# Kernel optimization log

Measured on AMD Instinct MI355X. Metric: run time of the kernel, lower is better.

The kernel has to match this reference:

```python
import jax, jax.numpy as jnp
import numpy as np

NUM_HEADS_LIST = [8, 16]
HIDDEN_SIZE_LIST = [1024, 2048]
NUM_HEADS_KV = 8
MAX_HIDDEN = max(HIDDEN_SIZE_LIST)
B, T = 4, 1024
NEG = -1e9


def _rope_cos_sin(position_ids, head_dim, dtype):
    # HF-style RoPE: inv_freq over even dims, emb = cat(freqs, freqs)
    inv_freq = 1.0 / (10000.0 ** (jnp.arange(0, head_dim, 2, dtype=jnp.float32) / head_dim))
    freqs = position_ids.astype(jnp.float32)[..., None] * inv_freq  # (B,T,d/2)
    emb = jnp.concatenate([freqs, freqs], axis=-1)                  # (B,T,d)
    # unsqueeze head dim -> (B,1,T,d)
    return jnp.cos(emb).astype(dtype)[:, None], jnp.sin(emb).astype(dtype)[:, None]


def _rotate_half(x):
    d = x.shape[-1] // 2
    return jnp.concatenate([-x[..., d:], x[..., :d]], axis=-1)


def setup_inputs() -> dict:
    key = jax.random.key(0)
    k1, k2, k3, k4 = jax.random.split(key, 4)
    q_m = jax.random.normal(k1, (B, T, MAX_HIDDEN), dtype=jnp.float32)
    k_m = jax.random.normal(k2, (B, T, MAX_HIDDEN), dtype=jnp.float32)
    v_m = jax.random.normal(k3, (B, T, MAX_HIDDEN), dtype=jnp.float32)
    weights = jax.random.uniform(k4, (len(NUM_HEADS_LIST) * len(HIDDEN_SIZE_LIST),), dtype=jnp.float32)
    weights = weights / jnp.sum(weights)
    causal = jnp.tril(jnp.ones((T, T), dtype=bool))
    attention_mask = jnp.broadcast_to(
        jnp.where(causal, 0.0, NEG).astype(jnp.float32)[None, None], (B, 1, T, T)
    )
    position_ids = jnp.broadcast_to(jnp.arange(T, dtype=jnp.int64)[None], (B, T))
    return {"q_m": q_m, "k_m": k_m, "v_m": v_m, "weights": weights,
            "attention_mask": attention_mask, "position_ids": position_ids}


def reference(q_m, k_m, v_m, weights, attention_mask, position_ids):
    b, t, _ = q_m.shape
    dtype = q_m.dtype
    out = jnp.zeros((b, t, MAX_HIDDEN), dtype)
    l = 0
    for h in NUM_HEADS_LIST:
        d_max = MAX_HIDDEN // h  # padded head dim for this head-count config
        q_mix = jnp.zeros((b, h, t, d_max), dtype)
        k_mix = jnp.zeros((b, NUM_HEADS_KV, t, d_max), dtype)
        v_mix = jnp.zeros((b, NUM_HEADS_KV, t, d_max), dtype)
        for e in HIDDEN_SIZE_LIST:
            d = e // h
            q = q_m[:, :, :e].reshape(b, t, h, d).transpose(0, 2, 1, 3)                  # (b,h,t,d)
            k = k_m[:, :, :d * NUM_HEADS_KV].reshape(b, t, NUM_HEADS_KV, d).transpose(0, 2, 1, 3)
            v = v_m[:, :, :d * NUM_HEADS_KV].reshape(b, t, NUM_HEADS_KV, d).transpose(0, 2, 1, 3)
            cos, sin = _rope_cos_sin(position_ids, d, dtype)
            q = q * cos + _rotate_half(q) * sin
            k = k * cos + _rotate_half(k) * sin
            pad = ((0, 0), (0, 0), (0, 0), (0, d_max - d))
            w = weights[l]
            q_mix = q_mix + w * jnp.pad(q, pad)
            k_mix = k_mix + w * jnp.pad(k, pad)
            v_mix = v_mix + w * jnp.pad(v, pad)
            l += 1
        # GQA: repeat kv heads to match h
        n_rep = h // NUM_HEADS_KV
        kr = jnp.repeat(k_mix, n_rep, axis=1)
        vr = jnp.repeat(v_mix, n_rep, axis=1)
        scale = 1.0 / np.sqrt(d_max).astype(np.float32)
        scores = jnp.einsum('bhqd,bhkd->bhqk', q_mix, kr) * scale
        scores = scores + attention_mask[:, :, :, :t]
        att = jax.nn.softmax(scores, axis=-1)
        y = jnp.einsum('bhqk,bhkd->bhqd', att, vr)
        y = y.transpose(0, 2, 1, 3).reshape(b, t, h * d_max)  # h*d_max == MAX_HIDDEN
        out = out + y
    return out
```

## Files before the change

### kernel.cpp

```cpp
#include <hip/hip_runtime.h>
#include <math.h>

#define B_   4
#define T_   1024
#define MAXH 2048
#define NKV  8

typedef unsigned int uint;
typedef unsigned short ushort;
typedef __attribute__((ext_vector_type(8))) short bf16x8;
typedef __attribute__((ext_vector_type(4))) float f32x4;

__device__ __forceinline__ ushort f2bf(float f) {
    uint u = __float_as_uint(f);
    u += 0x7fffu + ((u >> 16) & 1u);
    return (ushort)(u >> 16);
}

template<int H1>
__global__ __launch_bounds__(256) void mixqk_fused(
    const float* __restrict__ src, ushort* __restrict__ dst0,
    ushort* __restrict__ dst1, const float* __restrict__ wts)
{
    __shared__ float L[2048];
    const int bt = blockIdx.x;
    const int t = bt & (T_ - 1), b = bt >> 10;
    const float* row = src + (size_t)bt * MAXH;
    const int tid = threadIdx.x;
#pragma unroll
    for (int i = 0; i < 2; i++) {
        int idx = tid + i * 256;
        *(float4*)&L[idx * 4] = *(const float4*)&row[idx * 4];
    }
    __syncthreads();
    const float w0s = wts[0], w0b = wts[1], w1s = wts[2], w1b = wts[3];
    const float tf = (float)t;
    constexpr float LG = 13.287712379549449f;

#pragma unroll
    for (int i = 0; i < 4; i++) {
        int p = tid + i * 256;
        int hh = p >> 7, jh = p & 127;
        float ab = tf * exp2f((float)jh * (-2.f * LG / 256.f));
        float sb = __sinf(ab), cb = __cosf(ab);
        float x0 = L[hh * 256 + jh], x1 = L[hh * 256 + jh + 128];
        float v0 = w0b * (x0 * cb - x1 * sb);
        float v1 = w0b * (x1 * cb + x0 * sb);
        float as = tf * exp2f((float)(jh & 63) * (-2.f * LG / 128.f));
        float ss = __sinf(as), cs = __cosf(as);
        float y  = L[hh * 128 + jh];
        float yr = (jh < 64) ? -L[hh * 128 + jh + 64] : L[hh * 128 + jh - 64];
        v0 += w0s * (y * cs + yr * ss);
        ushort* d0 = dst0 + (((size_t)b * 8 + hh) * T_ + t) * 256;
        d0[jh] = f2bf(v0); d0[jh + 128] = f2bf(v1);
    }
#pragma unroll
    for (int i = 0; i < H1 / 4; i++) {
        int p = tid + i * 256;
        int h = p >> 6, jh = p & 63;
        float ab = tf * exp2f((float)jh * (-2.f * LG / 128.f));
        float sb = __sinf(ab), cb = __cosf(ab);
        float x0 = L[h * 128 + jh], x1 = L[h * 128 + jh + 64];
        float v0 = w1b * (x0 * cb - x1 * sb);
        float v1 = w1b * (x1 * cb + x0 * sb);
        float as = tf * exp2f((float)(jh & 31) * (-2.f * LG / 64.f));
        float ss = __sinf(as), cs = __cosf(as);
        float y  = L[h * 64 + jh];
        float yr = (jh < 32) ? -L[h * 64 + jh + 32] : L[h * 64 + jh - 32];
        v0 += w1s * (y * cs + yr * ss);
        ushort* d1 = dst1 + (((size_t)b * H1 + h) * T_ + t) * 128;
        d1[jh] = f2bf(v0); d1[jh + 64] = f2bf(v1);
    }
}

template<int DMAX>
__global__ __launch_bounds__(256) void mixv_t(
    const float* __restrict__ src, ushort* __restrict__ dst,
    const float* __restrict__ wts, int wsi, int wbi)
{
    constexpr int DS = DMAX / 2;
    constexpr int DDN = DMAX / 32;
    __shared__ ushort tile[32][33];
    int bid = blockIdx.x;
    int dd = bid % DDN;  bid /= DDN;
    int tt = bid & 31;   int bk = bid >> 5;
    int b = bk >> 3, kh = bk & 7;
    int tid = threadIdx.x;
    float wb = wts[wbi], wsm = wts[wsi];

    int jloc = tid & 31;
    int j = dd * 32 + jloc;
#pragma unroll
    for (int p = 0; p < 4; p++) {
        int tl = (tid >> 5) + p * 8;
        const float* row = src + ((size_t)b * T_ + tt * 32 + tl) * MAXH;
        float v = wb * row[kh * DMAX + j];
        if (j < DS) v += wsm * row[kh * DS + j];
        tile[tl][jloc] = f2bf(v);
    }
    __syncthreads();
    int tl = tid & 31;
#pragma unroll
    for (int p = 0; p < 4; p++) {
        int jl = (tid >> 5) + p * 8;
        dst[((size_t)bk * DMAX + dd * 32 + jl) * T_ + tt * 32 + tl] = tile[tl][jl];
    }
}

template<int NC, int NSUB, int RS, int NQ>
__device__ __forceinline__ void attn_inst(
    const bf16x8* qf, f32x4* acc, f32x4* accl, ushort* ps,
    const ushort* lds, int ksbase, int vtbase,
    float scale2, int qw, int kt32, int qtr, int l16)
{
    const bool full = (kt32 + 31) <= qw;
    f32x4 s0[NQ], s1[NQ];
#pragma unroll
    for (int qi = 0; qi < NQ; qi++) { s0[qi] = (f32x4){0.f,0.f,0.f,0.f}; s1[qi] = (f32x4){0.f,0.f,0.f,0.f}; }

    __builtin_amdgcn_s_setprio(1);
#pragma unroll
    for (int c = 0; c < NC; c++) {
        int ch = ((c * 4 + qtr) ^ (l16 & 7)) * 8;
        bf16x8 k0 = *(const bf16x8*)&lds[ksbase + l16 * RS + ch];
        bf16x8 k1 = *(const bf16x8*)&lds[ksbase + (16 + l16) * RS + ch];
#pragma unroll
        for (int qi = 0; qi < NQ; qi++) {
            s0[qi] = __builtin_amdgcn_mfma_f32_16x16x32_bf16(qf[qi * NC + c], k0, s0[qi], 0, 0, 0);
            s1[qi] = __builtin_amdgcn_mfma_f32_16x16x32_bf16(qf[qi * NC + c], k1, s1[qi], 0, 0, 0);
        }
    }
    __builtin_amdgcn_s_setprio(0);

    bf16x8 pa[NQ];
#pragma unroll
    for (int qi = 0; qi < NQ; qi++) {
        float p0[4], p1[4];
#pragma unroll
        for (int rr = 0; rr < 4; rr++) {
            p0[rr] = exp2f(s0[qi][rr] * scale2);
            p1[rr] = exp2f(s1[qi][rr] * scale2);
            if (!full) {
                int qq = qw + qtr * 4 + rr;
                if (kt32 + l16 > qq)      p0[rr] = 0.f;
                if (kt32 + 16 + l16 > qq) p1[rr] = 0.f;
            }
        }
#pragma unroll
        for (int rr = 0; rr < 4; rr++) {
            int row = qtr * 4 + rr;
            ps[row * 32 + (((l16 >> 3) ^ (row & 3)) * 8) + (l16 & 7)]       = f2bf(p0[rr]);
            ps[row * 32 + (((2 + (l16 >> 3)) ^ (row & 3)) * 8) + (l16 & 7)] = f2bf(p1[rr]);
        }
        pa[qi] = *(const bf16x8*)&ps[l16 * 32 + ((qtr ^ (l16 & 3)) * 8)];
    }

    bf16x8 ones;
#pragma unroll
    for (int j = 0; j < 8; j++) ones[j] = (short)0x3f80;
    __builtin_amdgcn_s_setprio(1);
#pragma unroll
    for (int s = 0; s < NSUB; s++) {
        bf16x8 vb = *(const bf16x8*)&lds[vtbase + (s * 16 + l16) * 40 + qtr * 8];
#pragma unroll
        for (int qi = 0; qi < NQ; qi++)
            acc[qi * NSUB + s] = __builtin_amdgcn_mfma_f32_16x16x32_bf16(pa[qi], vb, acc[qi * NSUB + s], 0, 0, 0);
    }
#pragma unroll
    for (int qi = 0; qi < NQ; qi++)
        accl[qi] = __builtin_amdgcn_mfma_f32_16x16x32_bf16(pa[qi], ones, accl[qi], 0, 0, 0);
    __builtin_amdgcn_s_setprio(0);
}

__global__ __launch_bounds__(512, 2) void attn_fused(
    const ushort* __restrict__ qmix0, const ushort* __restrict__ kmix0, const ushort* __restrict__ vt0,
    const ushort* __restrict__ qmix1, const ushort* __restrict__ kmix1, const ushort* __restrict__ vt1,
    float* __restrict__ out)
{
    __shared__ alignas(16) ushort lds[31744];
    constexpr int KS0 = 0, KS1 = 8192, VT0 = 12288, VT1 = 22528, PS = 27648;

    const int bid = blockIdx.x;
    const int half = bid >> 8;
    const int ipair = (bid >> 5) & 7;
    const int idx = bid & 31;
    const int b = idx >> 3, kh = idx & 7;
    const int qt = half ? ipair : 15 - ipair;

    const int tid = threadIdx.x;
    const int wid = tid >> 6, lane = tid & 63;
    const int qtr = lane >> 4, l16 = lane & 15;
    const int cfg = wid >> 2;
    const int w4 = wid & 3;

    const ushort* kg0 = kmix0 + ((size_t)b * NKV + kh) * T_ * 256;
    const ushort* vg0 = vt0   + ((size_t)b * NKV + kh) * 256 * T_;
    const ushort* kg1 = kmix1 + ((size_t)b * NKV + kh) * T_ * 128;
    const ushort* vg1 = vt1   + ((size_t)b * NKV + kh) * 128 * T_;

    const int k0r0 = tid >> 5,         k0c0 = tid & 31;
    const int k0r1 = (tid + 512) >> 5, k0c1 = (tid + 512) & 31;
    const int v0d0 = tid >> 2,         v0c0 = tid & 3;
    const int v0d1 = (tid + 512) >> 2, v0c1 = (tid + 512) & 3;
    const int k1r = tid >> 4, k1c = tid & 15;
    const int v1d = tid >> 2, v1c = tid & 3;

    ushort* ps = &lds[PS + wid * 512];

    const int nkt = 2 * qt + 2;
    const int qw = qt * 64 + w4 * 16;

    bf16x8 qf[8];
    if (cfg == 0) {
        const ushort* qb = qmix0 + (((size_t)b * 8 + kh) * T_ + qw + l16) * 256 + qtr * 8;
#pragma unroll
        for (int c = 0; c < 8; c++) qf[c] = *(const bf16x8*)(qb + c * 32);
    } else {
#pragma unroll
        for (int hI = 0; hI < 2; hI++) {
            const ushort* qb = qmix1 + (((size_t)b * 16 + 2 * kh + hI) * T_ + qw + l16) * 128 + qtr * 8;
#pragma unroll
            for (int c = 0; c < 4; c++) qf[hI * 4 + c] = *(const bf16x8*)(qb + c * 32);
        }
    }

    f32x4 acc[16];
    f32x4 accl[2] = {{0.f,0.f,0.f,0.f},{0.f,0.f,0.f,0.f}};
#pragma unroll
    for (int s = 0; s < 16; s++) acc[s] = (f32x4){0.f,0.f,0.f,0.f};

    const float scale2_0 = 0.0625f * 1.4426950408889634f;
    const float scale2_1 = 0.08838834764831845f * 1.4426950408889634f;

    uint4 k0a, k0b, v0a, v0b, k1a, v1a;
#define ISSUE(kt_) do {                                                              \
        k0a = *(const uint4*)(kg0 + (size_t)((kt_) * 32 + k0r0) * 256 + k0c0 * 8);   \
        k0b = *(const uint4*)(kg0 + (size_t)((kt_) * 32 + k0r1) * 256 + k0c1 * 8);   \
        v0a = *(const uint4*)(vg0 + (size_t)v0d0 * T_ + (kt_) * 32 + v0c0 * 8);      \
        v0b = *(const uint4*)(vg0 + (size_t)v0d1 * T_ + (kt_) * 32 + v0c1 * 8);      \
        k1a = *(const uint4*)(kg1 + (size_t)((kt_) * 32 + k1r) * 128 + k1c * 8);     \
        v1a = *(const uint4*)(vg1 + (size_t)v1d * T_ + (kt_) * 32 + v1c * 8);        \
    } while (0)

    ISSUE(0);
    for (int kt = 0; kt < nkt; kt++) {
        asm volatile("s_barrier" ::: "memory");
        *(uint4*)&lds[KS0 + k0r0 * 256 + ((k0c0 ^ (k0r0 & 7)) * 8)] = k0a;
        *(uint4*)&lds[KS0 + k0r1 * 256 + ((k0c1 ^ (k0r1 & 7)) * 8)] = k0b;
        *(uint4*)&lds[VT0 + v0d0 * 40 + v0c0 * 8] = v0a;
        *(uint4*)&lds[VT0 + v0d1 * 40 + v0c1 * 8] = v0b;
        *(uint4*)&lds[KS1 + k1r * 128 + ((k1c ^ (k1r & 7)) * 8)] = k1a;
        *(uint4*)&lds[VT1 + v1d * 40 + v1c * 8] = v1a;
        if (kt + 1 < nkt) ISSUE(kt + 1);
        asm volatile("s_waitcnt lgkmcnt(0)" ::: "memory");
        asm volatile("s_barrier" ::: "memory");

        const int kt32 = kt * 32;
        if (kt32 > qw + 15) continue;

        if (cfg == 0) {
            attn_inst<8, 16, 256, 1>(qf, acc, accl, ps, lds, KS0, VT0,
                                     scale2_0, qw, kt32, qtr, l16);
        } else {
            attn_inst<4, 8, 128, 2>(qf, acc, accl, ps, lds, KS1, VT1,
                                    scale2_1, qw, kt32, qtr, l16);
        }
    }
#undef ISSUE

    if (cfg == 0) {
        float linv[4];
#pragma unroll
        for (int rr = 0; rr < 4; rr++) linv[rr] = 1.f / accl[0][rr];
        float* ob = out + ((size_t)b * T_ + qw) * MAXH + kh * 256;
#pragma unroll
        for (int s = 0; s < 16; s++)
#pragma unroll
            for (int rr = 0; rr < 4; rr++)
                ob[(size_t)(qtr * 4 + rr) * MAXH + s * 16 + l16] = acc[s][rr] * linv[rr];
    }
    __syncthreads();
    if (cfg == 1) {
        float linva[4], linvb[4];
#pragma unroll
        for (int rr = 0; rr < 4; rr++) { linva[rr] = 1.f / accl[0][rr]; linvb[rr] = 1.f / accl[1][rr]; }
        float* ob = out + ((size_t)b * T_ + qw) * MAXH + kh * 256;
#pragma unroll
        for (int s = 0; s < 8; s++)
#pragma unroll
            for (int rr = 0; rr < 4; rr++)
                ob[(size_t)(qtr * 4 + rr) * MAXH + s * 16 + l16] += acc[s][rr] * linva[rr];
#pragma unroll
        for (int s = 0; s < 8; s++)
#pragma unroll
            for (int rr = 0; rr < 4; rr++)
                ob[(size_t)(qtr * 4 + rr) * MAXH + 128 + s * 16 + l16] += acc[8 + s][rr] * linvb[rr];
    }
}

extern "C" void kernel_launch(void* const* d_in, const int* in_sizes, int n_in,
                              void* d_out, int out_size, void* d_ws, size_t ws_size,
                              hipStream_t stream) {
    const float* q_m = (const float*)d_in[0];
    const float* k_m = (const float*)d_in[1];
    const float* v_m = (const float*)d_in[2];
    const float* wts = (const float*)d_in[3];
    float* out = (float*)d_out;
    ushort* ws = (ushort*)d_ws;

    ushort* qmix0 = ws;
    ushort* kmix0 = ws + 8388608u;
    ushort* vt0   = ws + 16777216u;
    ushort* qmix1 = ws + 25165824u;
    ushort* kmix1 = ws + 33554432u;
    ushort* vt1   = ws + 37748736u;

    dim3 blk(256);
    mixqk_fused<16><<<4096, blk, 0, stream>>>(q_m, qmix0, qmix1, wts);
    mixqk_fused<8><<<4096, blk, 0, stream>>>(k_m, kmix0, kmix1, wts);
    mixv_t<256><<<8192, blk, 0, stream>>>(v_m, vt0, wts, 0, 1);
    mixv_t<128><<<4096, blk, 0, stream>>>(v_m, vt1, wts, 2, 3);

    attn_fused<<<dim3(512), dim3(512), 0, stream>>>(qmix0, kmix0, vt0, qmix1, kmix1, vt1, out);
}
```

Baseline: 142.2 us.

## Split attention per config into separate blocks with atomic output accumulation, fuse prep kernels

Merges the four mixing/transposing kernels into one launch that also zeroes the output buffer. The attention kernel is split so each 256-thread block handles only one head-count config rather than both, doubling the grid to 1024 blocks and cutting LDS use to allow three blocks per CU. The two configs' contributions are combined with float atomic adds into the zeroed output instead of ordered writes. The V LDS pitch also shrinks from 40 to 36. This trades fewer launches and better occupancy against extra atomic traffic, an output zeroing pass, and nondeterministic summation order.

```diff
diff --git a/kernel.cpp b/kernel.cpp
--- a/kernel.cpp
+++ b/kernel.cpp
@@ -18,12 +18,10 @@
 }
 
 template<int H1>
-__global__ __launch_bounds__(256) void mixqk_fused(
-    const float* __restrict__ src, ushort* __restrict__ dst0,
-    ushort* __restrict__ dst1, const float* __restrict__ wts)
-{
-    __shared__ float L[2048];
-    const int bt = blockIdx.x;
+__device__ __forceinline__ void mixqk_body(
+    int bt, const float* __restrict__ src, ushort* __restrict__ dst0,
+    ushort* __restrict__ dst1, const float* __restrict__ wts, float* L)
+{
     const int t = bt & (T_ - 1), b = bt >> 10;
     const float* row = src + (size_t)bt * MAXH;
     const int tid = threadIdx.x;
@@ -74,14 +72,12 @@
 }
 
 template<int DMAX>
-__global__ __launch_bounds__(256) void mixv_t(
-    const float* __restrict__ src, ushort* __restrict__ dst,
-    const float* __restrict__ wts, int wsi, int wbi)
+__device__ __forceinline__ void mixv_body(
+    int bid, const float* __restrict__ src, ushort* __restrict__ dst,
+    const float* __restrict__ wts, int wsi, int wbi, ushort* tile )
 {
     constexpr int DS = DMAX / 2;
     constexpr int DDN = DMAX / 32;
-    __shared__ ushort tile[32][33];
-    int bid = blockIdx.x;
     int dd = bid % DDN;  bid /= DDN;
     int tt = bid & 31;   int bk = bid >> 5;
     int b = bk >> 3, kh = bk & 7;
@@ -96,18 +92,43 @@
         const float* row = src + ((size_t)b * T_ + tt * 32 + tl) * MAXH;
         float v = wb * row[kh * DMAX + j];
         if (j < DS) v += wsm * row[kh * DS + j];
-        tile[tl][jloc] = f2bf(v);
+        tile[tl * 33 + jloc] = f2bf(v);
     }
     __syncthreads();
     int tl = tid & 31;
 #pragma unroll
     for (int p = 0; p < 4; p++) {
         int jl = (tid >> 5) + p * 8;
-        dst[((size_t)bk * DMAX + dd * 32 + jl) * T_ + tt * 32 + tl] = tile[tl][jl];
-    }
-}
-
-template<int NC, int NSUB, int RS, int NQ>
+        dst[((size_t)bk * DMAX + dd * 32 + jl) * T_ + tt * 32 + tl] = tile[tl * 33 + jl];
+    }
+}
+
+__global__ __launch_bounds__(256) void mix_all(
+    const float* __restrict__ q_m, const float* __restrict__ k_m, const float* __restrict__ v_m,
+    const float* __restrict__ wts, float* __restrict__ out,
+    ushort* qmix0, ushort* kmix0, ushort* vt0,
+    ushort* qmix1, ushort* kmix1, ushort* vt1)
+{
+    __shared__ float L[2048];
+    const int bid = blockIdx.x;
+    const int tid = threadIdx.x;
+    if (bid < 2048) {
+        float4 z = {0.f, 0.f, 0.f, 0.f};
+        float* ob = out + (size_t)bid * 4096;
+#pragma unroll
+        for (int i = 0; i < 4; i++) *(float4*)&ob[(tid + i * 256) * 4] = z;
+    } else if (bid < 6144) {
+        mixqk_body<16>(bid - 2048, q_m, qmix0, qmix1, wts, L);
+    } else if (bid < 10240) {
+        mixqk_body<8>(bid - 6144, k_m, kmix0, kmix1, wts, L);
+    } else if (bid < 18432) {
+        mixv_body<256>(bid - 10240, v_m, vt0, wts, 0, 1, (ushort*)L);
+    } else {
+        mixv_body<128>(bid - 18432, v_m, vt1, wts, 2, 3, (ushort*)L);
+    }
+}
+
+template<int NC, int NSUB, int RS, int NQ, int VP>
 __device__ __forceinline__ void attn_inst(
     const bf16x8* qf, f32x4* acc, f32x4* accl, ushort* ps,
     const ushort* lds, int ksbase, int vtbase,
@@ -161,7 +182,7 @@
     __builtin_amdgcn_s_setprio(1);
 #pragma unroll
     for (int s = 0; s < NSUB; s++) {
-        bf16x8 vb = *(const bf16x8*)&lds[vtbase + (s * 16 + l16) * 40 + qtr * 8];
+        bf16x8 vb = *(const bf16x8*)&lds[vtbase + (s * 16 + l16) * VP + qtr * 8];
 #pragma unroll
         for (int qi = 0; qi < NQ; qi++)
             acc[qi * NSUB + s] = __builtin_amdgcn_mfma_f32_16x16x32_bf16(pa[qi], vb, acc[qi * NSUB + s], 0, 0, 0);
@@ -172,129 +193,142 @@
     __builtin_amdgcn_s_setprio(0);
 }
 
-__global__ __launch_bounds__(512, 2) void attn_fused(
+__global__ __launch_bounds__(256, 3) void attn_sp(
     const ushort* __restrict__ qmix0, const ushort* __restrict__ kmix0, const ushort* __restrict__ vt0,
     const ushort* __restrict__ qmix1, const ushort* __restrict__ kmix1, const ushort* __restrict__ vt1,
     float* __restrict__ out)
 {
-    __shared__ alignas(16) ushort lds[31744];
-    constexpr int KS0 = 0, KS1 = 8192, VT0 = 12288, VT1 = 22528, PS = 27648;
+    __shared__ alignas(16) ushort lds[19456];
+    constexpr int PSOFF = 17408;
+    constexpr int VP = 36;
 
     const int bid = blockIdx.x;
-    const int half = bid >> 8;
-    const int ipair = (bid >> 5) & 7;
     const int idx = bid & 31;
     const int b = idx >> 3, kh = idx & 7;
-    const int qt = half ? ipair : 15 - ipair;
+    const int m = bid >> 5;
+    const int qt = 15 - (m >> 1);
+    const int cfg = m & 1;
 
     const int tid = threadIdx.x;
     const int wid = tid >> 6, lane = tid & 63;
     const int qtr = lane >> 4, l16 = lane & 15;
-    const int cfg = wid >> 2;
-    const int w4 = wid & 3;
-
-    const ushort* kg0 = kmix0 + ((size_t)b * NKV + kh) * T_ * 256;
-    const ushort* vg0 = vt0   + ((size_t)b * NKV + kh) * 256 * T_;
-    const ushort* kg1 = kmix1 + ((size_t)b * NKV + kh) * T_ * 128;
-    const ushort* vg1 = vt1   + ((size_t)b * NKV + kh) * 128 * T_;
-
-    const int k0r0 = tid >> 5,         k0c0 = tid & 31;
-    const int k0r1 = (tid + 512) >> 5, k0c1 = (tid + 512) & 31;
-    const int v0d0 = tid >> 2,         v0c0 = tid & 3;
-    const int v0d1 = (tid + 512) >> 2, v0c1 = (tid + 512) & 3;
-    const int k1r = tid >> 4, k1c = tid & 15;
-    const int v1d = tid >> 2, v1c = tid & 3;
-
-    ushort* ps = &lds[PS + wid * 512];
-
+    const int qw = qt * 64 + wid * 16;
     const int nkt = 2 * qt + 2;
-    const int qw = qt * 64 + w4 * 16;
-
-    bf16x8 qf[8];
+    ushort* ps = &lds[PSOFF + wid * 512];
+
+    const float scale2_0 = 0.0625f * 1.4426950408889634f;
+    const float scale2_1 = 0.08838834764831845f * 1.4426950408889634f;
+
     if (cfg == 0) {
-        const ushort* qb = qmix0 + (((size_t)b * 8 + kh) * T_ + qw + l16) * 256 + qtr * 8;
-#pragma unroll
-        for (int c = 0; c < 8; c++) qf[c] = *(const bf16x8*)(qb + c * 32);
+        const ushort* kg = kmix0 + ((size_t)b * NKV + kh) * T_ * 256;
+        const ushort* vg = vt0   + ((size_t)b * NKV + kh) * (size_t)256 * T_;
+        bf16x8 qf[8];
+        {
+            const ushort* qb = qmix0 + (((size_t)b * 8 + kh) * T_ + qw + l16) * 256 + qtr * 8;
+#pragma unroll
+            for (int c = 0; c < 8; c++) qf[c] = *(const bf16x8*)(qb + c * 32);
+        }
+        f32x4 acc[16];
+        f32x4 accl = {0.f,0.f,0.f,0.f};
+#pragma unroll
+        for (int s = 0; s < 16; s++) acc[s] = (f32x4){0.f,0.f,0.f,0.f};
+
+        uint4 kreg[4], vreg[4];
+#define ISSUE0(kt_) do {                                                                   \
+        _Pragma("unroll")                                                                  \
+        for (int i = 0; i < 4; i++) {                                                      \
+            int id = tid + i * 256;                                                        \
+            kreg[i] = *(const uint4*)(kg + (size_t)((kt_) * 32 + (id >> 5)) * 256 + (id & 31) * 8); \
+            vreg[i] = *(const uint4*)(vg + (size_t)(id >> 2) * T_ + (kt_) * 32 + (id & 3) * 8);     \
+        } } while (0)
+
+        ISSUE0(0);
+        for (int kt = 0; kt < nkt; kt++) {
+            asm volatile("s_barrier" ::: "memory");
+#pragma unroll
+            for (int i = 0; i < 4; i++) {
+                int id = tid + i * 256;
+                int kr = id >> 5, kc = id & 31;
+                *(uint4*)&lds[kr * 256 + ((kc ^ (kr & 7)) * 8)] = kreg[i];
+                *(uint4*)&lds[8192 + (id >> 2) * VP + (id & 3) * 8] = vreg[i];
+            }
+            if (kt + 1 < nkt) ISSUE0(kt + 1);
+            asm volatile("s_waitcnt lgkmcnt(0)" ::: "memory");
+            asm volatile("s_barrier" ::: "memory");
+
+            const int kt32 = kt * 32;
+            if (kt32 > qw + 15) continue;
+            attn_inst<8, 16, 256, 1, VP>(qf, acc, &accl, ps, lds, 0, 8192,
+                                         scale2_0, qw, kt32, qtr, l16);
+        }
+#undef ISSUE0
+        float linv[4];
+#pragma unroll
+        for (int rr = 0; rr < 4; rr++) linv[rr] = 1.f / accl[rr];
+        float* ob = out + ((size_t)b * T_ + qw) * MAXH + kh * 256;
+#pragma unroll
+        for (int s = 0; s < 16; s++)
+#pragma unroll
+            for (int rr = 0; rr < 4; rr++)
+                unsafeAtomicAdd(ob + (size_t)(qtr * 4 + rr) * MAXH + s * 16 + l16,
+                                acc[s][rr] * linv[rr]);
     } else {
+        const ushort* kg = kmix1 + ((size_t)b * NKV + kh) * T_ * 128;
+        const ushort* vg = vt1   + ((size_t)b * NKV + kh) * (size_t)128 * T_;
+        bf16x8 qf[8];
 #pragma unroll
         for (int hI = 0; hI < 2; hI++) {
             const ushort* qb = qmix1 + (((size_t)b * 16 + 2 * kh + hI) * T_ + qw + l16) * 128 + qtr * 8;
 #pragma unroll
             for (int c = 0; c < 4; c++) qf[hI * 4 + c] = *(const bf16x8*)(qb + c * 32);
         }
-    }
-
-    f32x4 acc[16];
-    f32x4 accl[2] = {{0.f,0.f,0.f,0.f},{0.f,0.f,0.f,0.f}};
-#pragma unroll
-    for (int s = 0; s < 16; s++) acc[s] = (f32x4){0.f,0.f,0.f,0.f};
-
-    const float scale2_0 = 0.0625f * 1.4426950408889634f;
-    const float scale2_1 = 0.08838834764831845f * 1.4426950408889634f;
-
-    uint4 k0a, k0b, v0a, v0b, k1a, v1a;
-#define ISSUE(kt_) do {                                                              \
-        k0a = *(const uint4*)(kg0 + (size_t)((kt_) * 32 + k0r0) * 256 + k0c0 * 8);   \
-        k0b = *(const uint4*)(kg0 + (size_t)((kt_) * 32 + k0r1) * 256 + k0c1 * 8);   \
-        v0a = *(const uint4*)(vg0 + (size_t)v0d0 * T_ + (kt_) * 32 + v0c0 * 8);      \
-        v0b = *(const uint4*)(vg0 + (size_t)v0d1 * T_ + (kt_) * 32 + v0c1 * 8);      \
-        k1a = *(const uint4*)(kg1 + (size_t)((kt_) * 32 + k1r) * 128 + k1c * 8);     \
-        v1a = *(const uint4*)(vg1 + (size_t)v1d * T_ + (kt_) * 32 + v1c * 8);        \
-    } while (0)
-
-    ISSUE(0);
-    for (int kt = 0; kt < nkt; kt++) {
-        asm volatile("s_barrier" ::: "memory");
-        *(uint4*)&lds[KS0 + k0r0 * 256 + ((k0c0 ^ (k0r0 & 7)) * 8)] = k0a;
-        *(uint4*)&lds[KS0 + k0r1 * 256 + ((k0c1 ^ (k0r1 & 7)) * 8)] = k0b;
-        *(uint4*)&lds[VT0 + v0d0 * 40 + v0c0 * 8] = v0a;
-        *(uint4*)&lds[VT0 + v0d1 * 40 + v0c1 * 8] = v0b;
-        *(uint4*)&lds[KS1 + k1r * 128 + ((k1c ^ (k1r & 7)) * 8)] = k1a;
-        *(uint4*)&lds[VT1 + v1d * 40 + v1c * 8] = v1a;
-        if (kt + 1 < nkt) ISSUE(kt + 1);
-        asm volatile("s_waitcnt lgkmcnt(0)" ::: "memory");
-        asm volatile("s_barrier" ::: "memory");
-
-        const int kt32 = kt * 32;
-        if (kt32 > qw + 15) continue;
-
-        if (cfg == 0) {
-            attn_inst<8, 16, 256, 1>(qf, acc, accl, ps, lds, KS0, VT0,
-                                     scale2_0, qw, kt32, qtr, l16);
-        } else {
-            attn_inst<4, 8, 128, 2>(qf, acc, accl, ps, lds, KS1, VT1,
-                                    scale2_1, qw, kt32, qtr, l16);
-        }
-    }
-#undef ISSUE
-
-    if (cfg == 0) {
-        float linv[4];
-#pragma unroll
-        for (int rr = 0; rr < 4; rr++) linv[rr] = 1.f / accl[0][rr];
-        float* ob = out + ((size_t)b * T_ + qw) * MAXH + kh * 256;
-#pragma unroll
-        for (int s = 0; s < 16; s++)
-#pragma unroll
-            for (int rr = 0; rr < 4; rr++)
-                ob[(size_t)(qtr * 4 + rr) * MAXH + s * 16 + l16] = acc[s][rr] * linv[rr];
-    }
-    __syncthreads();
-    if (cfg == 1) {
-        float linva[4], linvb[4];
-#pragma unroll
-        for (int rr = 0; rr < 4; rr++) { linva[rr] = 1.f / accl[0][rr]; linvb[rr] = 1.f / accl[1][rr]; }
-        float* ob = out + ((size_t)b * T_ + qw) * MAXH + kh * 256;
-#pragma unroll
-        for (int s = 0; s < 8; s++)
-#pragma unroll
-            for (int rr = 0; rr < 4; rr++)
-                ob[(size_t)(qtr * 4 + rr) * MAXH + s * 16 + l16] += acc[s][rr] * linva[rr];
-#pragma unroll
-        for (int s = 0; s < 8; s++)
-#pragma unroll
-            for (int rr = 0; rr < 4; rr++)
-                ob[(size_t)(qtr * 4 + rr) * MAXH + 128 + s * 16 + l16] += acc[8 + s][rr] * linvb[rr];
+        f32x4 acc[16];
+        f32x4 accl[2] = {{0.f,0.f,0.f,0.f},{0.f,0.f,0.f,0.f}};
+#pragma unroll
+        for (int s = 0; s < 16; s++) acc[s] = (f32x4){0.f,0.f,0.f,0.f};
+
+        uint4 kreg[2], vreg[2];
+#define ISSUE1(kt_) do {                                                                   \
+        _Pragma("unroll")                                                                  \
+        for (int i = 0; i < 2; i++) {                                                      \
+            int id = tid + i * 256;                                                        \
+            kreg[i] = *(const uint4*)(kg + (size_t)((kt_) * 32 + (id >> 4)) * 128 + (id & 15) * 8); \
+            vreg[i] = *(const uint4*)(vg + (size_t)(id >> 2) * T_ + (kt_) * 32 + (id & 3) * 8);     \
+        } } while (0)
+
+        ISSUE1(0);
+        for (int kt = 0; kt < nkt; kt++) {
+            asm volatile("s_barrier" ::: "memory");
+#pragma unroll
+            for (int i = 0; i < 2; i++) {
+                int id = tid + i * 256;
+                int kr = id >> 4, kc = id & 15;
+                *(uint4*)&lds[kr * 128 + ((kc ^ (kr & 7)) * 8)] = kreg[i];
+                *(uint4*)&lds[4096 + (id >> 2) * VP + (id & 3) * 8] = vreg[i];
+            }
+            if (kt + 1 < nkt) ISSUE1(kt + 1);
+            asm volatile("s_waitcnt lgkmcnt(0)" ::: "memory");
+            asm volatile("s_barrier" ::: "memory");
+
+            const int kt32 = kt * 32;
+            if (kt32 > qw + 15) continue;
+            attn_inst<4, 8, 128, 2, VP>(qf, acc, accl, ps, lds, 0, 4096,
+                                        scale2_1, qw, kt32, qtr, l16);
+        }
+#undef ISSUE1
+#pragma unroll
+        for (int hI = 0; hI < 2; hI++) {
+            float linv[4];
+#pragma unroll
+            for (int rr = 0; rr < 4; rr++) linv[rr] = 1.f / accl[hI][rr];
+            float* ob = out + ((size_t)b * T_ + qw) * MAXH + kh * 256 + hI * 128;
+#pragma unroll
+            for (int s = 0; s < 8; s++)
+#pragma unroll
+                for (int rr = 0; rr < 4; rr++)
+                    unsafeAtomicAdd(ob + (size_t)(qtr * 4 + rr) * MAXH + s * 16 + l16,
+                                    acc[hI * 8 + s][rr] * linv[rr]);
+        }
     }
 }
 
@@ -315,11 +349,7 @@
     ushort* kmix1 = ws + 33554432u;
     ushort* vt1   = ws + 37748736u;
 
-    dim3 blk(256);
-    mixqk_fused<16><<<4096, blk, 0, stream>>>(q_m, qmix0, qmix1, wts);
-    mixqk_fused<8><<<4096, blk, 0, stream>>>(k_m, kmix0, kmix1, wts);
-    mixv_t<256><<<8192, blk, 0, stream>>>(v_m, vt0, wts, 0, 1);
-    mixv_t<128><<<4096, blk, 0, stream>>>(v_m, vt1, wts, 2, 3);
-
-    attn_fused<<<dim3(512), dim3(512), 0, stream>>>(qmix0, kmix0, vt0, qmix1, kmix1, vt1, out);
-}
+    mix_all<<<dim3(22528), dim3(256), 0, stream>>>(q_m, k_m, v_m, wts, out,
+                                                   qmix0, kmix0, vt0, qmix1, kmix1, vt1);
+    attn_sp<<<dim3(1024), dim3(256), 0, stream>>>(qmix0, kmix0, vt0, qmix1, kmix1, vt1, out);
+}
```

New measurement: 274.0 us. 92.7% more time.
